# Performance work log

Hardware: AMD Instinct MI355X
Metric: run time of the kernel (lower is better)

## Reference

```python
import jax, jax.numpy as jnp
import numpy as np

OUT_FEATURES = 512
IN_FEATURES = 512


def _unfold_tt(G1, G2):
    # G1: (1, do0, r, di0), G2: (r, do1, 1, di1)
    # einsum 'abcd,cefg->abefdg' then reshape -> (out_features, in_features)
    W = jnp.einsum('abcd,cefg->abefdg', G1, G2)
    return W.reshape(OUT_FEATURES, IN_FEATURES)


def setup_inputs() -> dict:
    key = jax.random.key(0)
    ks = jax.random.split(key, 5)
    std = np.sqrt(2.0 / IN_FEATURES).astype(np.float32)
    x = jax.random.normal(ks[0], (8, 4096, 2 * IN_FEATURES), dtype=jnp.float32)
    G1_R = jax.random.uniform(ks[1], (1, 32, 4, 32), jnp.float32, -std, std)
    G2_R = jax.random.uniform(ks[2], (4, 16, 1, 16), jnp.float32, -std, std)
    G1_I = jax.random.uniform(ks[3], (1, 32, 4, 32), jnp.float32, -std, std)
    G2_I = jax.random.uniform(ks[4], (4, 16, 1, 16), jnp.float32, -std, std)
    bias_real = jnp.zeros((OUT_FEATURES,), jnp.float32)
    bias_imag = jnp.zeros((OUT_FEATURES,), jnp.float32)
    return {"x": x, "G1_R": G1_R, "G2_R": G2_R, "G1_I": G1_I, "G2_I": G2_I,
            "bias_real": bias_real, "bias_imag": bias_imag}


def reference(x, G1_R, G2_R, G1_I, G2_I, bias_real, bias_imag):
    W_real = _unfold_tt(G1_R, G2_R)  # (out, in)
    W_imag = _unfold_tt(G1_I, G2_I)
    x_real, x_imag = jnp.split(x, 2, axis=-1)
    # F.linear(x, W, b) = x @ W.T + b
    out_real = x_real @ W_real.T - x_imag @ W_imag.T + bias_real
    out_imag = x_real @ W_imag.T + x_imag @ W_real.T + bias_imag
    return jnp.concatenate([out_real, out_imag], axis=-1)
```

## Files before the change

kernel.cpp:

```cpp
#include <hip/hip_runtime.h>
#include <hip/hip_bf16.h>
#include <stdint.h>


typedef _Float16 half8 __attribute__((ext_vector_type(8)));
typedef _Float16 half4v __attribute__((ext_vector_type(4)));
typedef float f32x4 __attribute__((ext_vector_type(4)));

typedef __attribute__((address_space(3))) void* lds_ptr_t;
typedef const __attribute__((address_space(1))) void* gbl_ptr_t;

__device__ __forceinline__ void gload_lds16(const void* g, void* s) {
  __builtin_amdgcn_global_load_lds((gbl_ptr_t)g, (lds_ptr_t)s, 16, 0, 0);
}

#define BARF() asm volatile("s_barrier" ::: "memory")
#define LGKM0() asm volatile("s_waitcnt lgkmcnt(0)" ::: "memory")
#define VMC6() asm volatile("s_waitcnt vmcnt(6)" ::: "memory")
#define VMC0() asm volatile("s_waitcnt vmcnt(0)" ::: "memory")
#define PRIO1() __builtin_amdgcn_s_setprio(1)
#define PRIO0() __builtin_amdgcn_s_setprio(0)


__global__ void build_bt(const float* __restrict__ G1R, const float* __restrict__ G2R,
                         const float* __restrict__ G1I, const float* __restrict__ G2I,
                         _Float16* __restrict__ BTimg) {
  int idx = blockIdx.x * 256 + threadIdx.x;
  int kcol = idx & 63;
  int row  = (idx >> 6) & 255;
  int kt   = (idx >> 14) & 15;
  int nt   = idx >> 18;
  int n = nt * 256 + row;
  int k = kt * 64 + kcol;
  int o = n & 511, i = k & 511;
  bool imagOut = n >= 512, kHi = k >= 512;
  const float* G1; const float* G2; float sign = 1.0f;
  if (imagOut == kHi) { G1 = G1R; G2 = G2R; }
  else { G1 = G1I; G2 = G2I; if (!imagOut) sign = -1.0f; }
  int b = o >> 4, e = o & 15, d = i >> 4, g = i & 15;
  float w = 0.0f;
#pragma unroll
  for (int c = 0; c < 4; ++c)
    w += G1[b * 128 + c * 32 + d] * G2[c * 256 + e * 16 + g];
  size_t byteoff = ((size_t)(nt * 16 + kt) << 15) + (size_t)row * 128
                 + ((kcol * 2) ^ ((row & 7) << 4));
  *(_Float16*)((char*)BTimg + byteoff) = (_Float16)(sign * w);
}

__global__ __launch_bounds__(256) void build_at(const float* __restrict__ A,
                                                _Float16* __restrict__ Aimg) {
  const int tid = threadIdx.x;
  const int kt = blockIdx.x & 15, mt = blockIdx.x >> 4;
  const float* src = A + (size_t)mt * 256 * 1024 + kt * 64;
  char* dst = (char*)Aimg + ((size_t)(mt * 16 + kt) << 15);
  const int cg = tid & 15;
  const int rb = tid >> 4;
#pragma unroll
  for (int r = 0; r < 16; ++r) {
    int row = rb + r * 16;
    float4 v = *(const float4*)(src + (size_t)row * 1024 + cg * 4);
    half4v h = { (_Float16)v.x, (_Float16)v.y, (_Float16)v.z, (_Float16)v.w };
    *(half4v*)(dst + row * 128 + ((cg * 8) ^ ((row & 7) << 4))) = h;
  }
}

__global__ __launch_bounds__(512, 2) void tt_gemm(
    const _Float16* __restrict__ Aimg, const _Float16* __restrict__ Bimg,
    const float* __restrict__ bias_r, const float* __restrict__ bias_i,
    float* __restrict__ C) {
  __shared__ __align__(16) _Float16 Als[2][16384];
  __shared__ __align__(16) _Float16 Bls[2][16384];

  const int tid = threadIdx.x;
  const int bid = blockIdx.x;
  const int bid2 = (bid & 7) * 64 + (bid >> 3);
  const int mt = bid2 >> 2, nt = bid2 & 3;

  const int lane = tid & 63, wid = tid >> 6;
  const int wm = wid >> 2, wn = wid & 3;
  const int lr = lane & 15, lq = lane >> 4;

  f32x4 acc[8][4] = {};
  half8 afr0[4][2], afr1[4][2], bfr0[2][2], bfr1[2][2];

  const char* Abase = (const char*)Aimg + ((size_t)mt << 19);
  const char* Bbase = (const char*)Bimg + ((size_t)nt << 19);
  const int qoff = wid * 1024 + lane * 16;
  const int qdst = wid * 1024;

  auto stageQ = [&](const char* base, int t, int q, _Float16* buf) {
    gload_lds16(base + ((size_t)t << 15) + (q << 13) + qoff,
                (char*)buf + (q << 13) + qdst);
  };
  auto lda = [&](const _Float16* buf, int mh, half8 (&af)[4][2]) {
#pragma unroll
    for (int mf = 0; mf < 4; ++mf)
#pragma unroll
      for (int kk = 0; kk < 2; ++kk) {
        int row = wm * 128 + mh * 64 + mf * 16 + lr;
        int byte = row * 128 + ((kk * 64 + lq * 16) ^ ((row & 7) << 4));
        af[mf][kk] = *(const half8*)((const char*)buf + byte);
      }
  };
  auto ldb = [&](const _Float16* buf, int nh, half8 (&bf)[2][2]) {
#pragma unroll
    for (int j = 0; j < 2; ++j)
#pragma unroll
      for (int kk = 0; kk < 2; ++kk) {
        int row = wn * 64 + (nh * 2 + j) * 16 + lr;
        int byte = row * 128 + ((kk * 64 + lq * 16) ^ ((row & 7) << 4));
        bf[j][kk] = *(const half8*)((const char*)buf + byte);
      }
  };
  auto mmaq = [&](half8 (&af)[4][2], half8 (&bf)[2][2], int mb, int nb) {
#pragma unroll
    for (int mf = 0; mf < 4; ++mf)
#pragma unroll
      for (int j = 0; j < 2; ++j)
#pragma unroll
        for (int kk = 0; kk < 2; ++kk)
          acc[mb + mf][nb + j] = __builtin_amdgcn_mfma_f32_16x16x32_f16(
              af[mf][kk], bf[j][kk], acc[mb + mf][nb + j], 0, 0, 0);
  };

  _Float16* A0 = Als[0]; _Float16* A1 = Als[1];
  _Float16* B0 = Bls[0]; _Float16* B1 = Bls[1];

#pragma unroll
  for (int q = 0; q < 4; ++q) stageQ(Abase, 0, q, A0);
#pragma unroll
  for (int q = 0; q < 4; ++q) stageQ(Bbase, 0, q, B0);
  stageQ(Abase, 1, 0, A1); stageQ(Abase, 1, 2, A1);
  stageQ(Bbase, 1, 0, B1); stageQ(Bbase, 1, 1, B1);
  stageQ(Bbase, 1, 2, B1); stageQ(Bbase, 1, 3, B1);
  VMC6();
  BARF();

  for (int i = 0; i < 8; ++i) {
    const int t1 = 2 * i + 1, t2 = 2 * i + 2, t3 = 2 * i + 3;
    const bool pf = (i < 7);
    lda(A0, 0, afr0); ldb(B0, 0, bfr0);
    stageQ(Abase, t1, 1, A1); stageQ(Abase, t1, 3, A1);
    BARF(); LGKM0(); PRIO1(); mmaq(afr0, bfr0, 0, 0); PRIO0(); BARF();
    ldb(B0, 1, bfr1);
    if (pf) { stageQ(Abase, t2, 0, A0); stageQ(Abase, t2, 2, A0); }
    BARF(); LGKM0(); PRIO1(); mmaq(afr0, bfr1, 0, 2); PRIO0(); BARF();
    lda(A0, 1, afr1);
    if (pf) { stageQ(Bbase, t2, 0, B0); stageQ(Bbase, t2, 1, B0); }
    BARF(); LGKM0(); PRIO1(); mmaq(afr1, bfr1, 4, 2); PRIO0(); BARF();
    if (pf) { stageQ(Bbase, t2, 2, B0); stageQ(Bbase, t2, 3, B0); }
    BARF(); LGKM0(); PRIO1(); mmaq(afr1, bfr0, 4, 0); PRIO0();
    if (pf) { VMC6(); } else { VMC0(); }
    BARF();
    lda(A1, 0, afr0); ldb(B1, 0, bfr0);
    if (pf) { stageQ(Abase, t2, 1, A0); stageQ(Abase, t2, 3, A0); }
    BARF(); LGKM0(); PRIO1(); mmaq(afr0, bfr0, 0, 0); PRIO0(); BARF();
    ldb(B1, 1, bfr1);
    if (pf) { stageQ(Abase, t3, 0, A1); stageQ(Abase, t3, 2, A1); }
    BARF(); LGKM0(); PRIO1(); mmaq(afr0, bfr1, 0, 2); PRIO0(); BARF();
    lda(A1, 1, afr1);
    if (pf) { stageQ(Bbase, t3, 0, B1); stageQ(Bbase, t3, 1, B1); }
    BARF(); LGKM0(); PRIO1(); mmaq(afr1, bfr1, 4, 2); PRIO0(); BARF();
    if (pf) { stageQ(Bbase, t3, 2, B1); stageQ(Bbase, t3, 3, B1); }
    BARF(); LGKM0(); PRIO1(); mmaq(afr1, bfr0, 4, 0); PRIO0();
    if (pf) { VMC6(); }
    BARF();
  }

  const int row0 = mt * 256, col0 = nt * 256;
#pragma unroll
  for (int fn = 0; fn < 4; ++fn) {
    int col = col0 + wn * 64 + fn * 16 + lr;
    float bias = (col < 512) ? bias_r[col] : bias_i[col - 512];
#pragma unroll
    for (int fm = 0; fm < 8; ++fm) {
      int r0 = row0 + wm * 128 + (fm >> 2) * 64 + (fm & 3) * 16 + lq * 4;
#pragma unroll
      for (int r = 0; r < 4; ++r)
        C[(size_t)(r0 + r) * 1024 + col] = acc[fm][fn][r] + bias;
    }
  }
}

extern "C" void kernel_launch(void* const* d_in, const int* in_sizes, int n_in,
                              void* d_out, int out_size, void* d_ws, size_t ws_size,
                              hipStream_t stream) {
  const float* x   = (const float*)d_in[0];
  const float* G1R = (const float*)d_in[1];
  const float* G2R = (const float*)d_in[2];
  const float* G1I = (const float*)d_in[3];
  const float* G2I = (const float*)d_in[4];
  const float* br  = (const float*)d_in[5];
  const float* bi  = (const float*)d_in[6];
  float* out = (float*)d_out;

  _Float16* Bimg = (_Float16*)d_ws;
  _Float16* Aimg = (_Float16*)((char*)d_ws + (2u << 20));

  build_bt<<<4096, 256, 0, stream>>>(G1R, G2R, G1I, G2I, Bimg);
  build_at<<<2048, 256, 0, stream>>>(x, Aimg);
  tt_gemm<<<512, 512, 0, stream>>>(Aimg, Bimg, br, bi, out);
}
```

Before: 129.4 us.

## Replace fine-grained ping-pong schedule with whole-tile double-buffered main loop

Swaps the staggered quarter-tile staging, where each k-tile was split into four MFMA phases with barriers around each, for a simple loop. Each iteration reads all A/B fragments for the tile, issues the global-to-LDS prefetch two tiles ahead into the same buffer, then runs all 64 MFMAs. This cuts barrier count and scheduling overhead, but holds more fragment registers live (afr[8][2], bfr[4][2]) and overlaps loads with compute less finely. That could raise register pressure at 2 waves per SIMD and leave more LDS-read latency exposed.

```diff
diff --git a/kernel.cpp b/kernel.cpp
--- a/kernel.cpp
+++ b/kernel.cpp
@@ -16,7 +16,7 @@
 
 #define BARF() asm volatile("s_barrier" ::: "memory")
 #define LGKM0() asm volatile("s_waitcnt lgkmcnt(0)" ::: "memory")
-#define VMC6() asm volatile("s_waitcnt vmcnt(6)" ::: "memory")
+#define VMC8() asm volatile("s_waitcnt vmcnt(8)" ::: "memory")
 #define VMC0() asm volatile("s_waitcnt vmcnt(0)" ::: "memory")
 #define PRIO1() __builtin_amdgcn_s_setprio(1)
 #define PRIO0() __builtin_amdgcn_s_setprio(0)
@@ -81,90 +81,68 @@
   const int lr = lane & 15, lq = lane >> 4;
 
   f32x4 acc[8][4] = {};
-  half8 afr0[4][2], afr1[4][2], bfr0[2][2], bfr1[2][2];
+  half8 afr[8][2];
+  half8 bfr[4][2];
 
   const char* Abase = (const char*)Aimg + ((size_t)mt << 19);
   const char* Bbase = (const char*)Bimg + ((size_t)nt << 19);
   const int qoff = wid * 1024 + lane * 16;
-  const int qdst = wid * 1024;
 
-  auto stageQ = [&](const char* base, int t, int q, _Float16* buf) {
-    gload_lds16(base + ((size_t)t << 15) + (q << 13) + qoff,
-                (char*)buf + (q << 13) + qdst);
+  auto stageT = [&](int t, _Float16* Abuf, _Float16* Bbuf) {
+    const char* sa = Abase + ((size_t)t << 15) + qoff;
+    const char* sb = Bbase + ((size_t)t << 15) + qoff;
+#pragma unroll
+    for (int q = 0; q < 4; ++q)
+      gload_lds16(sa + q * 8192, (char*)Abuf + q * 8192 + wid * 1024);
+#pragma unroll
+    for (int q = 0; q < 4; ++q)
+      gload_lds16(sb + q * 8192, (char*)Bbuf + q * 8192 + wid * 1024);
   };
-  auto lda = [&](const _Float16* buf, int mh, half8 (&af)[4][2]) {
+  auto fragReads = [&](const _Float16* Abuf, const _Float16* Bbuf) {
 #pragma unroll
-    for (int mf = 0; mf < 4; ++mf)
+    for (int mf = 0; mf < 8; ++mf)
 #pragma unroll
       for (int kk = 0; kk < 2; ++kk) {
-        int row = wm * 128 + mh * 64 + mf * 16 + lr;
+        int row = wm * 128 + mf * 16 + lr;
         int byte = row * 128 + ((kk * 64 + lq * 16) ^ ((row & 7) << 4));
-        af[mf][kk] = *(const half8*)((const char*)buf + byte);
+        afr[mf][kk] = *(const half8*)((const char*)Abuf + byte);
+      }
+#pragma unroll
+    for (int j = 0; j < 4; ++j)
+#pragma unroll
+      for (int kk = 0; kk < 2; ++kk) {
+        int row = wn * 64 + j * 16 + lr;
+        int byte = row * 128 + ((kk * 64 + lq * 16) ^ ((row & 7) << 4));
+        bfr[j][kk] = *(const half8*)((const char*)Bbuf + byte);
       }
   };
-  auto ldb = [&](const _Float16* buf, int nh, half8 (&bf)[2][2]) {
+  auto mmaAll = [&]() {
 #pragma unroll
-    for (int j = 0; j < 2; ++j)
+    for (int mf = 0; mf < 8; ++mf)
 #pragma unroll
-      for (int kk = 0; kk < 2; ++kk) {
-        int row = wn * 64 + (nh * 2 + j) * 16 + lr;
-        int byte = row * 128 + ((kk * 64 + lq * 16) ^ ((row & 7) << 4));
-        bf[j][kk] = *(const half8*)((const char*)buf + byte);
-      }
-  };
-  auto mmaq = [&](half8 (&af)[4][2], half8 (&bf)[2][2], int mb, int nb) {
-#pragma unroll
-    for (int mf = 0; mf < 4; ++mf)
-#pragma unroll
-      for (int j = 0; j < 2; ++j)
+      for (int j = 0; j < 4; ++j)
 #pragma unroll
         for (int kk = 0; kk < 2; ++kk)
-          acc[mb + mf][nb + j] = __builtin_amdgcn_mfma_f32_16x16x32_f16(
-              af[mf][kk], bf[j][kk], acc[mb + mf][nb + j], 0, 0, 0);
+          acc[mf][j] = __builtin_amdgcn_mfma_f32_16x16x32_f16(
+              afr[mf][kk], bfr[j][kk], acc[mf][j], 0, 0, 0);
   };
 
-  _Float16* A0 = Als[0]; _Float16* A1 = Als[1];
-  _Float16* B0 = Bls[0]; _Float16* B1 = Bls[1];
-
-#pragma unroll
-  for (int q = 0; q < 4; ++q) stageQ(Abase, 0, q, A0);
-#pragma unroll
-  for (int q = 0; q < 4; ++q) stageQ(Bbase, 0, q, B0);
-  stageQ(Abase, 1, 0, A1); stageQ(Abase, 1, 2, A1);
-  stageQ(Bbase, 1, 0, B1); stageQ(Bbase, 1, 1, B1);
-  stageQ(Bbase, 1, 2, B1); stageQ(Bbase, 1, 3, B1);
-  VMC6();
+  stageT(0, Als[0], Bls[0]);
+  stageT(1, Als[1], Bls[1]);
+  VMC8();
   BARF();
 
-  for (int i = 0; i < 8; ++i) {
-    const int t1 = 2 * i + 1, t2 = 2 * i + 2, t3 = 2 * i + 3;
-    const bool pf = (i < 7);
-    lda(A0, 0, afr0); ldb(B0, 0, bfr0);
-    stageQ(Abase, t1, 1, A1); stageQ(Abase, t1, 3, A1);
-    BARF(); LGKM0(); PRIO1(); mmaq(afr0, bfr0, 0, 0); PRIO0(); BARF();
-    ldb(B0, 1, bfr1);
-    if (pf) { stageQ(Abase, t2, 0, A0); stageQ(Abase, t2, 2, A0); }
-    BARF(); LGKM0(); PRIO1(); mmaq(afr0, bfr1, 0, 2); PRIO0(); BARF();
-    lda(A0, 1, afr1);
-    if (pf) { stageQ(Bbase, t2, 0, B0); stageQ(Bbase, t2, 1, B0); }
-    BARF(); LGKM0(); PRIO1(); mmaq(afr1, bfr1, 4, 2); PRIO0(); BARF();
-    if (pf) { stageQ(Bbase, t2, 2, B0); stageQ(Bbase, t2, 3, B0); }
-    BARF(); LGKM0(); PRIO1(); mmaq(afr1, bfr0, 4, 0); PRIO0();
-    if (pf) { VMC6(); } else { VMC0(); }
+#pragma unroll 2
+  for (int t = 0; t < 16; ++t) {
+    const int c = t & 1;
+    fragReads(Als[c], Bls[c]);
+    LGKM0();
     BARF();
-    lda(A1, 0, afr0); ldb(B1, 0, bfr0);
-    if (pf) { stageQ(Abase, t2, 1, A0); stageQ(Abase, t2, 3, A0); }
-    BARF(); LGKM0(); PRIO1(); mmaq(afr0, bfr0, 0, 0); PRIO0(); BARF();
-    ldb(B1, 1, bfr1);
-    if (pf) { stageQ(Abase, t3, 0, A1); stageQ(Abase, t3, 2, A1); }
-    BARF(); LGKM0(); PRIO1(); mmaq(afr0, bfr1, 0, 2); PRIO0(); BARF();
-    lda(A1, 1, afr1);
-    if (pf) { stageQ(Bbase, t3, 0, B1); stageQ(Bbase, t3, 1, B1); }
-    BARF(); LGKM0(); PRIO1(); mmaq(afr1, bfr1, 4, 2); PRIO0(); BARF();
-    if (pf) { stageQ(Bbase, t3, 2, B1); stageQ(Bbase, t3, 3, B1); }
-    BARF(); LGKM0(); PRIO1(); mmaq(afr1, bfr0, 4, 0); PRIO0();
-    if (pf) { VMC6(); }
-    BARF();
+    if (t < 14) stageT(t + 2, Als[c], Bls[c]);
+    PRIO1(); mmaAll(); PRIO0();
+    if (t < 14) { VMC8(); }
+    else if (t == 14) { VMC0(); }
+    if (t < 15) BARF();
   }
 
   const int row0 = mt * 256, col0 = nt * 256;
@@ -174,7 +152,7 @@
     float bias = (col < 512) ? bias_r[col] : bias_i[col - 512];
 #pragma unroll
     for (int fm = 0; fm < 8; ++fm) {
-      int r0 = row0 + wm * 128 + (fm >> 2) * 64 + (fm & 3) * 16 + lq * 4;
+      int r0 = row0 + wm * 128 + fm * 16 + lq * 4;
 #pragma unroll
       for (int r = 0; r < 4; ++r)
         C[(size_t)(r0 + r) * 1024 + col] = acc[fm][fn][r] + bias;
```

Result: no change. 130.4 us (+0.8%).
